# Optimization experiments

Hardware: AMD Instinct MI355X
Metric: run time of the kernel (lower is better)

## Reference

```python
import jax, jax.numpy as jnp
import numpy as np

EMBED_DIM = 1024
LATEN_DIM = 1024
B, S = 4, 2048


def setup_inputs() -> dict:
    key = jax.random.key(0)
    k1, k2, k3, k4, k5 = jax.random.split(key, 5)
    xq = jax.random.normal(k1, (B, S, EMBED_DIM), dtype=jnp.float32)
    xk = jax.random.normal(k2, (B, S, EMBED_DIM), dtype=jnp.float32)
    xv = jax.random.normal(k3, (B, S, EMBED_DIM), dtype=jnp.float32)
    # Linear weight init similar to torch default scale
    bound = 1.0 / np.sqrt(EMBED_DIM)
    Wq = jax.random.uniform(k4, (EMBED_DIM, EMBED_DIM), minval=-bound, maxval=bound, dtype=jnp.float32)
    bq = jax.random.uniform(k5, (EMBED_DIM,), minval=-bound, maxval=bound, dtype=jnp.float32)
    # causal mask: 1 => masked (future positions)
    att_mask = jnp.triu(jnp.ones((S, S), dtype=jnp.int32), k=1)
    return {"xq": xq, "xk": xk, "xv": xv, "Wq": Wq, "bq": bq, "att_mask": att_mask}


def reference(xq, xk, xv, Wq, bq, att_mask):
    scale = LATEN_DIM ** (-0.5)
    # Faithful to source: linearQ is applied to all three inputs.
    Q = jnp.einsum('bsd,ed->bse', xq, Wq) + bq
    K = jnp.einsum('bsd,ed->bse', xk, Wq) + bq
    V = jnp.einsum('bsd,ed->bse', xv, Wq) + bq
    scores = jnp.einsum('bqe,bke->bqk', Q, K) * scale  # [B, S, S]
    scores = jnp.where(att_mask == 1, -jnp.inf, scores)
    probs = jax.nn.softmax(scores, axis=-1)
    return jnp.einsum('bqk,bke->bqe', probs, V)
```

## Files before the change

kernel.cpp:

```cpp
#include <hip/hip_runtime.h>
#include <hip/hip_bf16.h>
#include <stdint.h>


typedef __attribute__((ext_vector_type(8))) short bf16x8;
typedef __attribute__((ext_vector_type(4))) float floatx4;

#define DEVI static __device__ __forceinline__

static constexpr int S_ = 2048;
static constexpr int E_ = 1024;
static constexpr int BATCH = 4;
static constexpr int N4X = 8192 * 1024 / 4;

DEVI unsigned short f2b(float f) {
  union { float f; unsigned u; } v; v.f = f;
  return (unsigned short)((v.u + 0x7FFFu + ((v.u >> 16) & 1u)) >> 16);
}

DEVI void async_load16(const void* g, void* l) {
  __builtin_amdgcn_global_load_lds(
      (__attribute__((address_space(1))) void*)(void*)(g),
      (__attribute__((address_space(3))) void*)(l),
      16, 0, 0);
}

DEVI void mfma_tile(const unsigned short* lsA, const unsigned short* lsB,
                    int m0, int n0, int lrow, int lk, floatx4 (&acc)[4][4]) {
  bf16x8 af[4], bfr[4];
#pragma unroll
  for (int i = 0; i < 4; ++i)
    af[i] = *(const bf16x8*)(lsA + (m0 + i * 16 + lrow) * 32 + lk);
#pragma unroll
  for (int i = 0; i < 4; ++i)
    bfr[i] = *(const bf16x8*)(lsB + (n0 + i * 16 + lrow) * 32 + lk);
#pragma unroll
  for (int mi = 0; mi < 4; ++mi)
#pragma unroll
    for (int ni = 0; ni < 4; ++ni)
      acc[mi][ni] = __builtin_amdgcn_mfma_f32_16x16x32_bf16(
          af[mi], bfr[ni], acc[mi][ni], 0, 0, 0);
}

DEVI void stage_bf16(const unsigned short* src, unsigned short* ls, int ld,
                     int tid) {
#pragma unroll
  for (int j = 0; j < 2; ++j) {
    int t = tid + j * 256, row = t >> 2, kk = (t & 3) << 3;
    async_load16(src + (size_t)row * ld + kk, ls + t * 8);
  }
}

__global__ void cvt_all(const float* __restrict__ xq,
                        const float* __restrict__ xk,
                        const float* __restrict__ xv,
                        const float* __restrict__ Wq,
                        unsigned short* __restrict__ Xb,
                        unsigned short* __restrict__ Wb) {
  int i = blockIdx.x * blockDim.x + threadIdx.x;
  const float4* src;
  ushort4* dst;
  if (i < 3 * N4X) {
    int seg = i / N4X, off = i - seg * N4X;
    const float* s = (seg == 0) ? xq : (seg == 1) ? xk : xv;
    src = (const float4*)s + off;
    dst = (ushort4*)(Xb + (size_t)seg * 8192 * 1024) + off;
  } else {
    int off = i - 3 * N4X;
    src = (const float4*)Wq + off;
    dst = (ushort4*)Wb + off;
  }
  float4 v = *src;
  ushort4 o;
  o.x = f2b(v.x); o.y = f2b(v.y); o.z = f2b(v.z); o.w = f2b(v.w);
  *dst = o;
}

__global__ __launch_bounds__(256) void gemm_qkv(
    const unsigned short* __restrict__ Xb, const unsigned short* __restrict__ Wb,
    const float* __restrict__ bias, unsigned short* __restrict__ Qb,
    unsigned short* __restrict__ Kb, unsigned short* __restrict__ Vt) {
  __shared__ __align__(16) unsigned short lsA[2][128 * 32];
  __shared__ __align__(16) unsigned short lsB[2][128 * 32];
  const int l = blockIdx.x;
  const int xcd = l & 7, i = l >> 3;
  const int bn = i & 7;
  const int bmg = xcd * 24 + (i >> 3);
  const int input = bmg / 64, bm = bmg % 64;
  const unsigned short* A = Xb + (size_t)bmg * 128 * 1024;
  const unsigned short* W = Wb + (size_t)bn * 128 * 1024;

  const int tid = threadIdx.x;
  const int lane = tid & 63, wave = tid >> 6;
  const int m0 = (wave >> 1) * 64, n0 = (wave & 1) * 64;
  const int lrow = lane & 15, lk = (lane >> 4) * 8;

  floatx4 acc[4][4] = {};

  for (int kt = 0; kt < 16; ++kt) {
    if (kt) __syncthreads();
    stage_bf16(A + kt * 64, lsA[0], 1024, tid);
    stage_bf16(A + kt * 64 + 32, lsA[1], 1024, tid);
    stage_bf16(W + kt * 64, lsB[0], 1024, tid);
    stage_bf16(W + kt * 64 + 32, lsB[1], 1024, tid);
    __syncthreads();
    mfma_tile(lsA[0], lsB[0], m0, n0, lrow, lk, acc);
    mfma_tile(lsA[1], lsB[1], m0, n0, lrow, lk, acc);
  }

  unsigned short* C = (input == 0) ? Qb : (input == 1) ? Kb : Vt;
  const int rb = (lane >> 4) * 4;
#pragma unroll
  for (int mi = 0; mi < 4; ++mi)
#pragma unroll
    for (int ni = 0; ni < 4; ++ni) {
      int gcol = bn * 128 + n0 + ni * 16 + lrow;
      float bv = bias[gcol];
#pragma unroll
      for (int r = 0; r < 4; ++r) {
        int grow = bm * 128 + m0 + mi * 16 + rb + r;
        unsigned short val = f2b(acc[mi][ni][r] + bv);
        if (input == 2) {
          int b = grow >> 11, s = grow & 2047;
          C[((size_t)b * 1024 + gcol) * 2048 + s] = val;
        } else {
          C[(size_t)grow * 1024 + gcol] = val;
        }
      }
    }
}

__global__ __launch_bounds__(256) void gemm_scores_exp(
    const unsigned short* __restrict__ Qb,
    const unsigned short* __restrict__ Kb, unsigned short* __restrict__ P,
    float* __restrict__ lsum) {
  const int l = blockIdx.x;
  const int xcd = l & 7, k = l >> 3;
  const int m = k & 7, gl = k >> 3;
  const int gg = xcd * 12 + gl;
  const int z = gg / 24, r0 = gg % 24;
  const int bm = (r0 < 8) ? r0 : 8 + ((r0 - 8) >> 1);
  const int bn = ((r0 < 8) ? 0 : ((r0 - 8) & 1)) * 8 + m;
  if (bn > bm) return;

  __shared__ __align__(16) unsigned short lsA[2][128 * 32];
  __shared__ __align__(16) unsigned short lsB[2][128 * 32];
  const unsigned short* A = Qb + ((size_t)z * S_ + bm * 128) * E_;
  const unsigned short* Bt = Kb + ((size_t)z * S_ + bn * 128) * E_;
  const int tid = threadIdx.x;
  const int lane = tid & 63, wave = tid >> 6;
  const int m0 = (wave >> 1) * 64, n0 = (wave & 1) * 64;
  const int lrow = lane & 15, lk = (lane >> 4) * 8;

  floatx4 acc[4][4] = {};
  for (int kt = 0; kt < 16; ++kt) {
    if (kt) __syncthreads();
    stage_bf16(A + kt * 64, lsA[0], E_, tid);
    stage_bf16(A + kt * 64 + 32, lsA[1], E_, tid);
    stage_bf16(Bt + kt * 64, lsB[0], E_, tid);
    stage_bf16(Bt + kt * 64 + 32, lsB[1], E_, tid);
    __syncthreads();
    mfma_tile(lsA[0], lsB[0], m0, n0, lrow, lk, acc);
    mfma_tile(lsA[1], lsB[1], m0, n0, lrow, lk, acc);
  }

  const int rb = (lane >> 4) * 4;
  const bool diag = (bm == bn);
#pragma unroll
  for (int mi = 0; mi < 4; ++mi)
#pragma unroll
    for (int r = 0; r < 4; ++r) {
      const int grow = bm * 128 + m0 + mi * 16 + rb + r;
      float rsum = 0.f;
#pragma unroll
      for (int ni = 0; ni < 4; ++ni) {
        const int gcol = bn * 128 + n0 + ni * 16 + lrow;
        float p = __expf(acc[mi][ni][r] * 0.03125f);
        if (diag && gcol > grow) p = 0.f;
        P[((size_t)z * S_ + grow) * S_ + gcol] = f2b(p);
        rsum += p;
      }
#pragma unroll
      for (int off = 1; off < 16; off <<= 1) rsum += __shfl_xor(rsum, off);
      if ((lane & 15) == 0) atomicAdd(&lsum[z * S_ + grow], rsum);
    }
}

__global__ __launch_bounds__(256) void gemm_pv(
    const unsigned short* __restrict__ Pb,
    const unsigned short* __restrict__ Vt, const float* __restrict__ lsum,
    float* __restrict__ Out) {
  __shared__ __align__(16) unsigned short lsA[2][128 * 32];
  __shared__ __align__(16) unsigned short lsB[2][128 * 32];
  const int l = blockIdx.x;
  const int xcd = l & 7, i = l >> 3;
  const int bn = i & 7, j = i >> 3;
  const int z = j >> 1;
  const int bm = (j & 1) ? xcd : 15 - xcd;

  const unsigned short* A = Pb + ((size_t)z * S_ + bm * 128) * S_;
  const unsigned short* Bt = Vt + ((size_t)z * E_ + bn * 128) * S_;
  float* C = Out + (size_t)z * S_ * E_;
  const int tid = threadIdx.x;
  const int lane = tid & 63, wave = tid >> 6;
  const int m0 = (wave >> 1) * 64, n0 = (wave & 1) * 64;
  const int lrow = lane & 15, lk = (lane >> 4) * 8;

  floatx4 acc[4][4] = {};
  const int nKK = (bm + 1) * 2;
  for (int kt = 0; kt < nKK; ++kt) {
    if (kt) __syncthreads();
    stage_bf16(A + kt * 64, lsA[0], S_, tid);
    stage_bf16(A + kt * 64 + 32, lsA[1], S_, tid);
    stage_bf16(Bt + kt * 64, lsB[0], S_, tid);
    stage_bf16(Bt + kt * 64 + 32, lsB[1], S_, tid);
    __syncthreads();
    mfma_tile(lsA[0], lsB[0], m0, n0, lrow, lk, acc);
    mfma_tile(lsA[1], lsB[1], m0, n0, lrow, lk, acc);
  }

  const int rb = (lane >> 4) * 4;
#pragma unroll
  for (int mi = 0; mi < 4; ++mi)
#pragma unroll
    for (int r = 0; r < 4; ++r) {
      const int grow = bm * 128 + m0 + mi * 16 + rb + r;
      const float inv = 1.0f / lsum[z * S_ + grow];
#pragma unroll
      for (int ni = 0; ni < 4; ++ni) {
        const int gcol = bn * 128 + n0 + ni * 16 + lrow;
        C[(size_t)grow * E_ + gcol] = acc[mi][ni][r] * inv;
      }
    }
}

extern "C" void kernel_launch(void* const* d_in, const int* in_sizes, int n_in,
                              void* d_out, int out_size, void* d_ws,
                              size_t ws_size, hipStream_t stream) {
  (void)in_sizes; (void)n_in; (void)out_size; (void)ws_size;
  const float* xq = (const float*)d_in[0];
  const float* xk = (const float*)d_in[1];
  const float* xv = (const float*)d_in[2];
  const float* Wq = (const float*)d_in[3];
  const float* bq = (const float*)d_in[4];
  float* out = (float*)d_out;

  unsigned short* base16 = (unsigned short*)d_ws;
  unsigned short* Xb = base16;
  unsigned short* P = base16;
  unsigned short* Wb = base16 + (size_t)24 * 1024 * 1024;
  unsigned short* Qb = Wb + (size_t)1024 * 1024;
  unsigned short* Kb = Qb + (size_t)8192 * 1024;
  unsigned short* Vt = Kb + (size_t)8192 * 1024;
  float* lsum = (float*)(Vt + (size_t)8192 * 1024);

  hipMemsetAsync(lsum, 0, BATCH * S_ * sizeof(float), stream);

  const int n4tot = 3 * N4X + 1024 * 1024 / 4;
  cvt_all<<<n4tot / 256, 256, 0, stream>>>(xq, xk, xv, Wq, Xb, Wb);

  gemm_qkv<<<1536, 256, 0, stream>>>(Xb, Wb, bq, Qb, Kb, Vt);
  gemm_scores_exp<<<768, 256, 0, stream>>>(Qb, Kb, P, lsum);
  gemm_pv<<<512, 256, 0, stream>>>(P, Vt, lsum, out);
}
```

Before: 304.9 us.

## Widen QKV GEMM tile to 128x256 and deepen K-step in attention GEMMs

The QKV projection GEMM now computes a 128x256 output tile per block, with each wave holding a 64x128 accumulator, and launches half as many blocks. This raises arithmetic intensity per A-tile load. The score and PV GEMMs now stage 128 K-elements per iteration instead of 64, halving the number of sync barriers per tile. The cost is more registers and more LDS per block (32 KB for QKV, 64 KB for the attention kernels), which may lower occupancy.

After: 355.0 us. 16.4% more time.

```diff
diff --git a/kernel.cpp b/kernel.cpp
--- a/kernel.cpp
+++ b/kernel.cpp
@@ -38,6 +38,24 @@
   for (int mi = 0; mi < 4; ++mi)
 #pragma unroll
     for (int ni = 0; ni < 4; ++ni)
+      acc[mi][ni] = __builtin_amdgcn_mfma_f32_16x16x32_bf16(
+          af[mi], bfr[ni], acc[mi][ni], 0, 0, 0);
+}
+
+DEVI void mfma_tile256(const unsigned short* lsA, const unsigned short* lsB,
+                       int m0, int n0, int lrow, int lk,
+                       floatx4 (&acc)[4][8]) {
+  bf16x8 af[4], bfr[8];
+#pragma unroll
+  for (int i = 0; i < 4; ++i)
+    af[i] = *(const bf16x8*)(lsA + (m0 + i * 16 + lrow) * 32 + lk);
+#pragma unroll
+  for (int i = 0; i < 8; ++i)
+    bfr[i] = *(const bf16x8*)(lsB + (n0 + i * 16 + lrow) * 32 + lk);
+#pragma unroll
+  for (int mi = 0; mi < 4; ++mi)
+#pragma unroll
+    for (int ni = 0; ni < 8; ++ni)
       acc[mi][ni] = __builtin_amdgcn_mfma_f32_16x16x32_bf16(
           af[mi], bfr[ni], acc[mi][ni], 0, 0, 0);
 }
@@ -81,31 +99,34 @@
     const float* __restrict__ bias, unsigned short* __restrict__ Qb,
     unsigned short* __restrict__ Kb, unsigned short* __restrict__ Vt) {
   __shared__ __align__(16) unsigned short lsA[2][128 * 32];
-  __shared__ __align__(16) unsigned short lsB[2][128 * 32];
+  __shared__ __align__(16) unsigned short lsB[2][256 * 32];
   const int l = blockIdx.x;
   const int xcd = l & 7, i = l >> 3;
-  const int bn = i & 7;
-  const int bmg = xcd * 24 + (i >> 3);
+  const int bn = i & 3;
+  const int bmg = xcd * 24 + (i >> 2);
   const int input = bmg / 64, bm = bmg % 64;
   const unsigned short* A = Xb + (size_t)bmg * 128 * 1024;
-  const unsigned short* W = Wb + (size_t)bn * 128 * 1024;
+  const unsigned short* W = Wb + (size_t)bn * 256 * 1024;
 
   const int tid = threadIdx.x;
   const int lane = tid & 63, wave = tid >> 6;
-  const int m0 = (wave >> 1) * 64, n0 = (wave & 1) * 64;
+  const int m0 = (wave >> 1) * 64, n0 = (wave & 1) * 128;
   const int lrow = lane & 15, lk = (lane >> 4) * 8;
 
-  floatx4 acc[4][4] = {};
+  floatx4 acc[4][8] = {};
 
   for (int kt = 0; kt < 16; ++kt) {
     if (kt) __syncthreads();
     stage_bf16(A + kt * 64, lsA[0], 1024, tid);
     stage_bf16(A + kt * 64 + 32, lsA[1], 1024, tid);
     stage_bf16(W + kt * 64, lsB[0], 1024, tid);
+    stage_bf16(W + (size_t)128 * 1024 + kt * 64, lsB[0] + 128 * 32, 1024, tid);
     stage_bf16(W + kt * 64 + 32, lsB[1], 1024, tid);
+    stage_bf16(W + (size_t)128 * 1024 + kt * 64 + 32, lsB[1] + 128 * 32, 1024,
+               tid);
     __syncthreads();
-    mfma_tile(lsA[0], lsB[0], m0, n0, lrow, lk, acc);
-    mfma_tile(lsA[1], lsB[1], m0, n0, lrow, lk, acc);
+    mfma_tile256(lsA[0], lsB[0], m0, n0, lrow, lk, acc);
+    mfma_tile256(lsA[1], lsB[1], m0, n0, lrow, lk, acc);
   }
 
   unsigned short* C = (input == 0) ? Qb : (input == 1) ? Kb : Vt;
@@ -113,8 +134,8 @@
 #pragma unroll
   for (int mi = 0; mi < 4; ++mi)
 #pragma unroll
-    for (int ni = 0; ni < 4; ++ni) {
-      int gcol = bn * 128 + n0 + ni * 16 + lrow;
+    for (int ni = 0; ni < 8; ++ni) {
+      int gcol = bn * 256 + n0 + ni * 16 + lrow;
       float bv = bias[gcol];
 #pragma unroll
       for (int r = 0; r < 4; ++r) {
@@ -143,8 +164,8 @@
   const int bn = ((r0 < 8) ? 0 : ((r0 - 8) & 1)) * 8 + m;
   if (bn > bm) return;
 
-  __shared__ __align__(16) unsigned short lsA[2][128 * 32];
-  __shared__ __align__(16) unsigned short lsB[2][128 * 32];
+  __shared__ __align__(16) unsigned short lsA[4][128 * 32];
+  __shared__ __align__(16) unsigned short lsB[4][128 * 32];
   const unsigned short* A = Qb + ((size_t)z * S_ + bm * 128) * E_;
   const unsigned short* Bt = Kb + ((size_t)z * S_ + bn * 128) * E_;
   const int tid = threadIdx.x;
@@ -153,15 +174,15 @@
   const int lrow = lane & 15, lk = (lane >> 4) * 8;
 
   floatx4 acc[4][4] = {};
-  for (int kt = 0; kt < 16; ++kt) {
+  for (int kt = 0; kt < 8; ++kt) {
     if (kt) __syncthreads();
-    stage_bf16(A + kt * 64, lsA[0], E_, tid);
-    stage_bf16(A + kt * 64 + 32, lsA[1], E_, tid);
-    stage_bf16(Bt + kt * 64, lsB[0], E_, tid);
-    stage_bf16(Bt + kt * 64 + 32, lsB[1], E_, tid);
+#pragma unroll
+    for (int j = 0; j < 4; ++j) stage_bf16(A + kt * 128 + j * 32, lsA[j], E_, tid);
+#pragma unroll
+    for (int j = 0; j < 4; ++j) stage_bf16(Bt + kt * 128 + j * 32, lsB[j], E_, tid);
     __syncthreads();
-    mfma_tile(lsA[0], lsB[0], m0, n0, lrow, lk, acc);
-    mfma_tile(lsA[1], lsB[1], m0, n0, lrow, lk, acc);
+#pragma unroll
+    for (int j = 0; j < 4; ++j) mfma_tile(lsA[j], lsB[j], m0, n0, lrow, lk, acc);
   }
 
   const int rb = (lane >> 4) * 4;
@@ -190,8 +211,8 @@
     const unsigned short* __restrict__ Pb,
     const unsigned short* __restrict__ Vt, const float* __restrict__ lsum,
     float* __restrict__ Out) {
-  __shared__ __align__(16) unsigned short lsA[2][128 * 32];
-  __shared__ __align__(16) unsigned short lsB[2][128 * 32];
+  __shared__ __align__(16) unsigned short lsA[4][128 * 32];
+  __shared__ __align__(16) unsigned short lsB[4][128 * 32];
   const int l = blockIdx.x;
   const int xcd = l & 7, i = l >> 3;
   const int bn = i & 7, j = i >> 3;
@@ -207,16 +228,19 @@
   const int lrow = lane & 15, lk = (lane >> 4) * 8;
 
   floatx4 acc[4][4] = {};
-  const int nKK = (bm + 1) * 2;
-  for (int kt = 0; kt < nKK; ++kt) {
+  const int nK = bm + 1;
+  for (int kt = 0; kt < nK; ++kt) {
     if (kt) __syncthreads();
-    stage_bf16(A + kt * 64, lsA[0], S_, tid);
-    stage_bf16(A + kt * 64 + 32, lsA[1], S_, tid);
-    stage_bf16(Bt + kt * 64, lsB[0], S_, tid);
-    stage_bf16(Bt + kt * 64 + 32, lsB[1], S_, tid);
+#pragma unroll
+    for (int j4 = 0; j4 < 4; ++j4)
+      stage_bf16(A + kt * 128 + j4 * 32, lsA[j4], S_, tid);
+#pragma unroll
+    for (int j4 = 0; j4 < 4; ++j4)
+      stage_bf16(Bt + kt * 128 + j4 * 32, lsB[j4], S_, tid);
     __syncthreads();
-    mfma_tile(lsA[0], lsB[0], m0, n0, lrow, lk, acc);
-    mfma_tile(lsA[1], lsB[1], m0, n0, lrow, lk, acc);
+#pragma unroll
+    for (int j4 = 0; j4 < 4; ++j4)
+      mfma_tile(lsA[j4], lsB[j4], m0, n0, lrow, lk, acc);
   }
 
   const int rb = (lane >> 4) * 4;
@@ -259,7 +283,7 @@
   const int n4tot = 3 * N4X + 1024 * 1024 / 4;
   cvt_all<<<n4tot / 256, 256, 0, stream>>>(xq, xk, xv, Wq, Xb, Wb);
 
-  gemm_qkv<<<1536, 256, 0, stream>>>(Xb, Wb, bq, Qb, Kb, Vt);
+  gemm_qkv<<<768, 256, 0, stream>>>(Xb, Wb, bq, Qb, Kb, Vt);
   gemm_scores_exp<<<768, 256, 0, stream>>>(Qb, Kb, P, lsum);
   gemm_pv<<<512, 256, 0, stream>>>(P, Vt, lsum, out);
 }
```

## Replace LDS-staged 128x128 tiles with single-wave 64x64 register-fed GEMMs

Applied to the files above, without the earlier changes.

All three GEMM kernels drop the shared-memory staging and block barriers. Each 64-thread workgroup now computes a 64x64 tile, loading MFMA fragments straight from global memory into registers with a two-stage software prefetch. The scores kernel enumerates only lower-triangular 64x64 tiles through a triangular index decode, which cuts masked work at finer grain, and the PV kernel uses 64-row causal K ranges. This removes LDS traffic and syncs, but each wave now fetches its own operands from global memory with no sharing across waves, which relies heavily on L2/MALL and risks being limited by memory bandwidth.

New measurement: 489.8 us. 1.61x slower.

```diff
diff --git a/kernel.cpp b/kernel.cpp
--- a/kernel.cpp
+++ b/kernel.cpp
@@ -18,36 +18,45 @@
   return (unsigned short)((v.u + 0x7FFFu + ((v.u >> 16) & 1u)) >> 16);
 }
 
-DEVI void async_load16(const void* g, void* l) {
-  __builtin_amdgcn_global_load_lds(
-      (__attribute__((address_space(1))) void*)(void*)(g),
-      (__attribute__((address_space(3))) void*)(l),
-      16, 0, 0);
-}
-
-DEVI void mfma_tile(const unsigned short* lsA, const unsigned short* lsB,
-                    int m0, int n0, int lrow, int lk, floatx4 (&acc)[4][4]) {
-  bf16x8 af[4], bfr[4];
+DEVI void load_frags(bf16x8 (&fr)[4], const unsigned short* __restrict__ base,
+                     const uint32_t (&off)[4], uint32_t k0) {
 #pragma unroll
   for (int i = 0; i < 4; ++i)
-    af[i] = *(const bf16x8*)(lsA + (m0 + i * 16 + lrow) * 32 + lk);
-#pragma unroll
-  for (int i = 0; i < 4; ++i)
-    bfr[i] = *(const bf16x8*)(lsB + (n0 + i * 16 + lrow) * 32 + lk);
+    fr[i] = *(const bf16x8*)(base + (off[i] + k0));
+}
+
+DEVI void mfma16(const bf16x8 (&a)[4], const bf16x8 (&b)[4],
+                 floatx4 (&acc)[4][4]) {
 #pragma unroll
   for (int mi = 0; mi < 4; ++mi)
 #pragma unroll
     for (int ni = 0; ni < 4; ++ni)
       acc[mi][ni] = __builtin_amdgcn_mfma_f32_16x16x32_bf16(
-          af[mi], bfr[ni], acc[mi][ni], 0, 0, 0);
-}
-
-DEVI void stage_bf16(const unsigned short* src, unsigned short* ls, int ld,
-                     int tid) {
-#pragma unroll
-  for (int j = 0; j < 2; ++j) {
-    int t = tid + j * 256, row = t >> 2, kk = (t & 3) << 3;
-    async_load16(src + (size_t)row * ld + kk, ls + t * 8);
+          a[mi], b[ni], acc[mi][ni], 0, 0, 0);
+}
+
+DEVI void core64(const unsigned short* __restrict__ A,
+                 const unsigned short* __restrict__ B, int lda, int ldb,
+                 int nSteps, int lane, floatx4 (&acc)[4][4]) {
+  const int lrow = lane & 15, lk8 = (lane >> 4) * 8;
+  uint32_t ao[4], bo[4];
+#pragma unroll
+  for (int i = 0; i < 4; ++i) {
+    ao[i] = (uint32_t)(i * 16 + lrow) * lda + lk8;
+    bo[i] = (uint32_t)(i * 16 + lrow) * ldb + lk8;
+  }
+  bf16x8 a0[4], b0[4], a1[4], b1[4];
+  load_frags(a0, A, ao, 0);
+  load_frags(b0, B, bo, 0);
+  for (int s = 0; s < nSteps; ++s) {
+    load_frags(a1, A, ao, (uint32_t)(2 * s + 1) * 32);
+    load_frags(b1, B, bo, (uint32_t)(2 * s + 1) * 32);
+    mfma16(a0, b0, acc);
+    if (s + 1 < nSteps) {
+      load_frags(a0, A, ao, (uint32_t)(2 * s + 2) * 32);
+      load_frags(b0, B, bo, (uint32_t)(2 * s + 2) * 32);
+    }
+    mfma16(a1, b1, acc);
   }
 }
 
@@ -76,49 +85,35 @@
   *dst = o;
 }
 
-__global__ __launch_bounds__(256) void gemm_qkv(
+__global__ __launch_bounds__(64) void gemm_qkv(
     const unsigned short* __restrict__ Xb, const unsigned short* __restrict__ Wb,
     const float* __restrict__ bias, unsigned short* __restrict__ Qb,
     unsigned short* __restrict__ Kb, unsigned short* __restrict__ Vt) {
-  __shared__ __align__(16) unsigned short lsA[2][128 * 32];
-  __shared__ __align__(16) unsigned short lsB[2][128 * 32];
   const int l = blockIdx.x;
-  const int xcd = l & 7, i = l >> 3;
-  const int bn = i & 7;
-  const int bmg = xcd * 24 + (i >> 3);
-  const int input = bmg / 64, bm = bmg % 64;
-  const unsigned short* A = Xb + (size_t)bmg * 128 * 1024;
-  const unsigned short* W = Wb + (size_t)bn * 128 * 1024;
-
-  const int tid = threadIdx.x;
-  const int lane = tid & 63, wave = tid >> 6;
-  const int m0 = (wave >> 1) * 64, n0 = (wave & 1) * 64;
-  const int lrow = lane & 15, lk = (lane >> 4) * 8;
+  const int xcd = l & 7, t = l >> 3;
+  const int bn64 = t & 15;
+  const int strip = (t >> 4) * 8 + xcd;
+  const int row0 = strip * 64;
+  const int input = row0 >> 13;
+  const unsigned short* A = Xb + (size_t)row0 * 1024;
+  const unsigned short* W = Wb + (size_t)bn64 * 64 * 1024;
+  const int lane = threadIdx.x;
 
   floatx4 acc[4][4] = {};
-
-  for (int kt = 0; kt < 16; ++kt) {
-    if (kt) __syncthreads();
-    stage_bf16(A + kt * 64, lsA[0], 1024, tid);
-    stage_bf16(A + kt * 64 + 32, lsA[1], 1024, tid);
-    stage_bf16(W + kt * 64, lsB[0], 1024, tid);
-    stage_bf16(W + kt * 64 + 32, lsB[1], 1024, tid);
-    __syncthreads();
-    mfma_tile(lsA[0], lsB[0], m0, n0, lrow, lk, acc);
-    mfma_tile(lsA[1], lsB[1], m0, n0, lrow, lk, acc);
-  }
+  core64(A, W, 1024, 1024, 16, lane, acc);
 
   unsigned short* C = (input == 0) ? Qb : (input == 1) ? Kb : Vt;
-  const int rb = (lane >> 4) * 4;
+  const int lrow = lane & 15, rb = (lane >> 4) * 4;
+  const int rloc = row0 & 8191;
 #pragma unroll
   for (int mi = 0; mi < 4; ++mi)
 #pragma unroll
     for (int ni = 0; ni < 4; ++ni) {
-      int gcol = bn * 128 + n0 + ni * 16 + lrow;
+      int gcol = bn64 * 64 + ni * 16 + lrow;
       float bv = bias[gcol];
 #pragma unroll
       for (int r = 0; r < 4; ++r) {
-        int grow = bm * 128 + m0 + mi * 16 + rb + r;
+        int grow = rloc + mi * 16 + rb + r;
         unsigned short val = f2b(acc[mi][ni][r] + bv);
         if (input == 2) {
           int b = grow >> 11, s = grow & 2047;
@@ -130,51 +125,37 @@
     }
 }
 
-__global__ __launch_bounds__(256) void gemm_scores_exp(
+__global__ __launch_bounds__(64) void gemm_scores_exp(
     const unsigned short* __restrict__ Qb,
     const unsigned short* __restrict__ Kb, unsigned short* __restrict__ P,
     float* __restrict__ lsum) {
   const int l = blockIdx.x;
-  const int xcd = l & 7, k = l >> 3;
-  const int m = k & 7, gl = k >> 3;
-  const int gg = xcd * 12 + gl;
-  const int z = gg / 24, r0 = gg % 24;
-  const int bm = (r0 < 8) ? r0 : 8 + ((r0 - 8) >> 1);
-  const int bn = ((r0 < 8) ? 0 : ((r0 - 8) & 1)) * 8 + m;
-  if (bn > bm) return;
-
-  __shared__ __align__(16) unsigned short lsA[2][128 * 32];
-  __shared__ __align__(16) unsigned short lsB[2][128 * 32];
-  const unsigned short* A = Qb + ((size_t)z * S_ + bm * 128) * E_;
-  const unsigned short* Bt = Kb + ((size_t)z * S_ + bn * 128) * E_;
-  const int tid = threadIdx.x;
-  const int lane = tid & 63, wave = tid >> 6;
-  const int m0 = (wave >> 1) * 64, n0 = (wave & 1) * 64;
-  const int lrow = lane & 15, lk = (lane >> 4) * 8;
+  const int xcd = l & 7, t = l >> 3;
+  const int g = xcd * 264 + t;
+  const int z = g / 528, r0 = g % 528;
+  int bm = (int)((sqrtf(8.0f * r0 + 1.0f) - 1.0f) * 0.5f);
+  while ((bm + 1) * (bm + 2) / 2 <= r0) ++bm;
+  while (bm * (bm + 1) / 2 > r0) --bm;
+  const int bn = r0 - bm * (bm + 1) / 2;
+
+  const unsigned short* A = Qb + ((size_t)z * S_ + bm * 64) * E_;
+  const unsigned short* Bt = Kb + ((size_t)z * S_ + bn * 64) * E_;
+  const int lane = threadIdx.x;
 
   floatx4 acc[4][4] = {};
-  for (int kt = 0; kt < 16; ++kt) {
-    if (kt) __syncthreads();
-    stage_bf16(A + kt * 64, lsA[0], E_, tid);
-    stage_bf16(A + kt * 64 + 32, lsA[1], E_, tid);
-    stage_bf16(Bt + kt * 64, lsB[0], E_, tid);
-    stage_bf16(Bt + kt * 64 + 32, lsB[1], E_, tid);
-    __syncthreads();
-    mfma_tile(lsA[0], lsB[0], m0, n0, lrow, lk, acc);
-    mfma_tile(lsA[1], lsB[1], m0, n0, lrow, lk, acc);
-  }
-
-  const int rb = (lane >> 4) * 4;
+  core64(A, Bt, E_, E_, 16, lane, acc);
+
+  const int lrow = lane & 15, rb = (lane >> 4) * 4;
   const bool diag = (bm == bn);
 #pragma unroll
   for (int mi = 0; mi < 4; ++mi)
 #pragma unroll
     for (int r = 0; r < 4; ++r) {
-      const int grow = bm * 128 + m0 + mi * 16 + rb + r;
+      const int grow = bm * 64 + mi * 16 + rb + r;
       float rsum = 0.f;
 #pragma unroll
       for (int ni = 0; ni < 4; ++ni) {
-        const int gcol = bn * 128 + n0 + ni * 16 + lrow;
+        const int gcol = bn * 64 + ni * 16 + lrow;
         float p = __expf(acc[mi][ni][r] * 0.03125f);
         if (diag && gcol > grow) p = 0.f;
         P[((size_t)z * S_ + grow) * S_ + gcol] = f2b(p);
@@ -182,53 +163,39 @@
       }
 #pragma unroll
       for (int off = 1; off < 16; off <<= 1) rsum += __shfl_xor(rsum, off);
-      if ((lane & 15) == 0) atomicAdd(&lsum[z * S_ + grow], rsum);
-    }
-}
-
-__global__ __launch_bounds__(256) void gemm_pv(
+      if (lrow == 0) atomicAdd(&lsum[z * S_ + grow], rsum);
+    }
+}
+
+__global__ __launch_bounds__(64) void gemm_pv(
     const unsigned short* __restrict__ Pb,
     const unsigned short* __restrict__ Vt, const float* __restrict__ lsum,
     float* __restrict__ Out) {
-  __shared__ __align__(16) unsigned short lsA[2][128 * 32];
-  __shared__ __align__(16) unsigned short lsB[2][128 * 32];
   const int l = blockIdx.x;
-  const int xcd = l & 7, i = l >> 3;
-  const int bn = i & 7, j = i >> 3;
-  const int z = j >> 1;
-  const int bm = (j & 1) ? xcd : 15 - xcd;
-
-  const unsigned short* A = Pb + ((size_t)z * S_ + bm * 128) * S_;
-  const unsigned short* Bt = Vt + ((size_t)z * E_ + bn * 128) * S_;
+  const int xcd = l & 7, t = l >> 3;
+  const int bn = t & 15, u = t >> 4;
+  const int p = u * 8 + xcd;
+  const int bm = 31 - (p >> 2);
+  const int z = p & 3;
+
+  const unsigned short* A = Pb + ((size_t)z * S_ + bm * 64) * S_;
+  const unsigned short* Bt = Vt + ((size_t)z * E_ + bn * 64) * S_;
   float* C = Out + (size_t)z * S_ * E_;
-  const int tid = threadIdx.x;
-  const int lane = tid & 63, wave = tid >> 6;
-  const int m0 = (wave >> 1) * 64, n0 = (wave & 1) * 64;
-  const int lrow = lane & 15, lk = (lane >> 4) * 8;
+  const int lane = threadIdx.x;
 
   floatx4 acc[4][4] = {};
-  const int nKK = (bm + 1) * 2;
-  for (int kt = 0; kt < nKK; ++kt) {
-    if (kt) __syncthreads();
-    stage_bf16(A + kt * 64, lsA[0], S_, tid);
-    stage_bf16(A + kt * 64 + 32, lsA[1], S_, tid);
-    stage_bf16(Bt + kt * 64, lsB[0], S_, tid);
-    stage_bf16(Bt + kt * 64 + 32, lsB[1], S_, tid);
-    __syncthreads();
-    mfma_tile(lsA[0], lsB[0], m0, n0, lrow, lk, acc);
-    mfma_tile(lsA[1], lsB[1], m0, n0, lrow, lk, acc);
-  }
-
-  const int rb = (lane >> 4) * 4;
+  core64(A, Bt, S_, S_, bm + 1, lane, acc);
+
+  const int lrow = lane & 15, rb = (lane >> 4) * 4;
 #pragma unroll
   for (int mi = 0; mi < 4; ++mi)
 #pragma unroll
     for (int r = 0; r < 4; ++r) {
-      const int grow = bm * 128 + m0 + mi * 16 + rb + r;
+      const int grow = bm * 64 + mi * 16 + rb + r;
       const float inv = 1.0f / lsum[z * S_ + grow];
 #pragma unroll
       for (int ni = 0; ni < 4; ++ni) {
-        const int gcol = bn * 128 + n0 + ni * 16 + lrow;
+        const int gcol = bn * 64 + ni * 16 + lrow;
         C[(size_t)grow * E_ + gcol] = acc[mi][ni][r] * inv;
       }
     }
@@ -259,7 +226,7 @@
   const int n4tot = 3 * N4X + 1024 * 1024 / 4;
   cvt_all<<<n4tot / 256, 256, 0, stream>>>(xq, xk, xv, Wq, Xb, Wb);
 
-  gemm_qkv<<<1536, 256, 0, stream>>>(Xb, Wb, bq, Qb, Kb, Vt);
-  gemm_scores_exp<<<768, 256, 0, stream>>>(Qb, Kb, P, lsum);
-  gemm_pv<<<512, 256, 0, stream>>>(P, Vt, lsum, out);
-}
+  gemm_qkv<<<6144, 64, 0, stream>>>(Xb, Wb, bq, Qb, Kb, Vt);
+  gemm_scores_exp<<<2112, 64, 0, stream>>>(Qb, Kb, P, lsum);
+  gemm_pv<<<2048, 64, 0, stream>>>(P, Vt, lsum, out);
+}
```
